# Performance work log

Hardware: AMD Instinct MI355X
Metric: run time of the kernel (lower is better)

## Reference

```python
import jax, jax.numpy as jnp
import numpy as np

WINDOW_SIZE = 11
SIGMA = 1.5
C1 = 0.01 ** 2
C2 = 0.03 ** 2


def _gaussian_window(window_size, sigma, channel):
    x = np.arange(window_size, dtype=np.float64)
    g = np.exp(-((x - window_size // 2) ** 2) / (2.0 * sigma ** 2))
    g = g / g.sum()
    w2d = np.outer(g, g).astype(np.float32)  # [K,K]
    # depthwise kernel: [C, 1, K, K] (OIHW with feature_group_count=C)
    return jnp.asarray(np.broadcast_to(w2d, (channel, 1, window_size, window_size)).copy())


def _depthwise_blur(x, window):
    pad = WINDOW_SIZE // 2
    return jax.lax.conv_general_dilated(
        x, window,
        window_strides=(1, 1),
        padding=[(pad, pad), (pad, pad)],
        feature_group_count=x.shape[1],
        dimension_numbers=('NCHW', 'OIHW', 'NCHW'))


def setup_inputs() -> dict:
    key = jax.random.key(0)
    k1, k2 = jax.random.split(key)
    shape = (16, 3, 512, 512)
    image = jax.random.uniform(k1, shape, dtype=jnp.float32)
    target = jax.random.uniform(k2, shape, dtype=jnp.float32)
    return {"image": image, "target": target}


def reference(image, target):
    channel = image.shape[1]
    window = _gaussian_window(WINDOW_SIZE, SIGMA, channel)

    mu1 = _depthwise_blur(image, window)
    mu2 = _depthwise_blur(target, window)
    mu1_sq = mu1 * mu1
    mu2_sq = mu2 * mu2
    mu1_mu2 = mu1 * mu2

    sigma1_sq = _depthwise_blur(image * image, window) - mu1_sq
    sigma2_sq = _depthwise_blur(target * target, window) - mu2_sq
    sigma12 = _depthwise_blur(image * target, window) - mu1_mu2

    ssim_map = ((2.0 * mu1_mu2 + C1) * (2.0 * sigma12 + C2)) / (
        (mu1_sq + mu2_sq + C1) * (sigma1_sq + sigma2_sq + C2))
    return 1.0 - jnp.mean(ssim_map)
```

## Files before the change

### kernel.cpp

```cpp
#include <hip/hip_runtime.h>
#include <hip/hip_fp16.h>
#include <math.h>


#define HH 512
#define WW 512
#define HW (HH*WW)
#define NPLANES 48
#define G_TILES 6
#define NBLOCKS 1024

typedef _Float16 f16x8 __attribute__((ext_vector_type(8)));
typedef _Float16 f16x4 __attribute__((ext_vector_type(4)));
typedef float f32x4 __attribute__((ext_vector_type(4)));

#define RAW_STRIDE 208
#define RAW_PLANE  9984
#define BUF_B      19968
#define LDS_TOTAL  39936

struct WParam { float A, B; };

__global__ void ssim_init_out(float* out) { out[0] = 1.0f; }

__device__ __forceinline__ void barrier_nodrain() {
    asm volatile("s_waitcnt lgkmcnt(0)" ::: "memory");
    __builtin_amdgcn_s_barrier();
    __builtin_amdgcn_sched_barrier(0);
}

__global__ __launch_bounds__(256, 4)
void ssim_mfma(const float* __restrict__ img, const float* __restrict__ tgt,
               float* __restrict__ out, WParam wp) {
    __shared__ alignas(16) char lds[LDS_TOTAL];
    __shared__ float wsum[4];

    const int tid  = threadIdx.x;
    const int wid  = tid >> 6;
    const int lane = tid & 63;
    const int cl   = lane & 15;
    const int am   = lane >> 4;

    const int it0 = tid,       ir0 = it0 / 10, ig0 = it0 - 10 * ir0;
    const int it1 = tid + 256, ir1 = it1 / 10, ig1 = it1 - 10 * ir1;
    const bool has1 = (tid < 164);

    float4 Xa[2], Xb[2], Ya[2], Yb[2];

    auto load_tile = [&](int tlin) {
        const int p   = tlin >> 7;
        const int rem = tlin & 127;
        const int R0  = (rem >> 3) * 32;
        const int C0  = (rem & 7) * 64;
        const float* ip = img + (size_t)p * HW;
        const float* tp = tgt + (size_t)p * HW;
        #pragma unroll
        for (int s = 0; s < 2; ++s) {
            if (s == 1 && !has1) break;
            int r   = s ? ir1 : ir0;
            int grp = s ? ig1 : ig0;
            int gr  = R0 - 5 + r;
            int gc0 = C0 - 8 + grp * 8;
            float4 xa = make_float4(0.f,0.f,0.f,0.f), xb = xa, ya = xa, yb = xa;
            if ((unsigned)gr < (unsigned)HH) {
                const float* xr = ip + (size_t)gr * WW;
                const float* yr = tp + (size_t)gr * WW;
                if ((unsigned)gc0 <= (unsigned)(WW - 4)) {
                    xa = *(const float4*)(xr + gc0);
                    ya = *(const float4*)(yr + gc0);
                }
                if ((unsigned)(gc0 + 4) <= (unsigned)(WW - 4)) {
                    xb = *(const float4*)(xr + gc0 + 4);
                    yb = *(const float4*)(yr + gc0 + 4);
                }
            }
            Xa[s] = xa; Xb[s] = xb; Ya[s] = ya; Yb[s] = yb;
        }
    };

    auto write_tile = [&](char* buf) {
        #pragma unroll
        for (int s = 0; s < 2; ++s) {
            if (s == 1 && !has1) break;
            int r   = s ? ir1 : ir0;
            int grp = s ? ig1 : ig0;
            f16x8 hx, hy;
            hx[0]=(_Float16)Xa[s].x; hx[1]=(_Float16)Xa[s].y;
            hx[2]=(_Float16)Xa[s].z; hx[3]=(_Float16)Xa[s].w;
            hx[4]=(_Float16)Xb[s].x; hx[5]=(_Float16)Xb[s].y;
            hx[6]=(_Float16)Xb[s].z; hx[7]=(_Float16)Xb[s].w;
            hy[0]=(_Float16)Ya[s].x; hy[1]=(_Float16)Ya[s].y;
            hy[2]=(_Float16)Ya[s].z; hy[3]=(_Float16)Ya[s].w;
            hy[4]=(_Float16)Yb[s].x; hy[5]=(_Float16)Yb[s].y;
            hy[6]=(_Float16)Yb[s].z; hy[7]=(_Float16)Yb[s].w;
            char* base = buf + r * RAW_STRIDE + grp * 16;
            *(f16x8*)(base + 0*RAW_PLANE) = hx;
            *(f16x8*)(base + 1*RAW_PLANE) = hy;
        }
    };

    const int base_t = blockIdx.x * G_TILES;
    load_tile(base_t);

    for (int i = tid; i < LDS_TOTAL / 4; i += 256)
        ((float*)lds)[i] = 0.f;

    f16x8 Bh;
    #pragma unroll
    for (int j = 0; j < 8; ++j) {
        int ih = 8*am + j - cl - 3;
        float t = (float)(ih - 5);
        Bh[j] = ((unsigned)ih <= 10u) ? (_Float16)(wp.A * exp2f(-wp.B*t*t))
                                      : (_Float16)0.f;
    }
    f16x4 Av1, Av2;
    #pragma unroll
    for (int j = 0; j < 4; ++j) {
        int k = 4*am + j;
        int i1 = k - cl;
        float t1 = (float)(i1 - 5);
        Av1[j] = ((unsigned)i1 <= 10u) ? (_Float16)(wp.A * exp2f(-wp.B*t1*t1))
                                       : (_Float16)0.f;
        int i2 = k + 16 - cl;
        float t2 = (float)(i2 - 5);
        Av2[j] = ((unsigned)i2 <= 10u) ? (_Float16)(wp.A * exp2f(-wp.B*t2*t2))
                                       : (_Float16)0.f;
    }
    __syncthreads();

    const float C1 = 1e-4f, C2 = 9e-4f;
    float lsum = 0.f;

    for (int g = 0; g < G_TILES; ++g) {
        char* buf = lds + (g & 1) * BUF_B;

        write_tile(buf);
        if (g + 1 < G_TILES) load_tile(base_t + g + 1);
        barrier_nodrain();

        {
            const int abase = cl * RAW_STRIDE + 32 * wid + am * 16;
            f16x8 hx3[3], hy3[3];
            #pragma unroll
            for (int mt = 0; mt < 3; ++mt) {
                hx3[mt] = *(const f16x8*)(buf + (16*mt) * RAW_STRIDE + abase);
                hy3[mt] = *(const f16x8*)(buf + RAW_PLANE + (16*mt) * RAW_STRIDE + abase);
            }

            f32x4 accv[4][2];
            #pragma unroll
            for (int q = 0; q < 4; ++q) {
                f32x4 Dh[3];
                #pragma unroll
                for (int mt = 0; mt < 3; ++mt) {
                    f16x8 A = (q == 0) ? hx3[mt]
                            : (q == 1) ? hy3[mt]
                            : (q == 2) ? (f16x8)(hx3[mt]*hx3[mt] + hy3[mt]*hy3[mt])
                                       : (f16x8)(hx3[mt]*hy3[mt]);
                    f32x4 zz = {0.f, 0.f, 0.f, 0.f};
                    Dh[mt] = __builtin_amdgcn_mfma_f32_16x16x32_f16(A, Bh, zz, 0, 0, 0);
                }
                #pragma unroll
                for (int mtv = 0; mtv < 2; ++mtv) {
                    f16x4 B1, B2;
                    #pragma unroll
                    for (int j = 0; j < 4; ++j) {
                        B1[j] = (_Float16)Dh[mtv][j];
                        B2[j] = (_Float16)Dh[mtv+1][j];
                    }
                    f32x4 zz = {0.f, 0.f, 0.f, 0.f};
                    f32x4 acc = __builtin_amdgcn_mfma_f32_16x16x16f16(Av2, B2, zz, 0, 0, 0);
                    accv[q][mtv] = __builtin_amdgcn_mfma_f32_16x16x16f16(Av1, B1, acc, 0, 0, 0);
                }
            }

            #pragma unroll
            for (int mtv = 0; mtv < 2; ++mtv) {
                #pragma unroll
                for (int j = 0; j < 4; ++j) {
                    float mu1 = accv[0][mtv][j], mu2 = accv[1][mtv][j];
                    float bss = accv[2][mtv][j], bxy = accv[3][mtv][j];
                    float mu1s = mu1*mu1, mu2s = mu2*mu2, mu12 = mu1*mu2;
                    float ssum = bss - mu1s - mu2s;
                    float s12  = bxy - mu12;
                    float num = (2.f*mu12 + C1) * (2.f*s12 + C2);
                    float den = (mu1s + mu2s + C1) * (ssum + C2);
                    lsum = fmaf(num, __builtin_amdgcn_rcpf(den), lsum);
                }
            }
        }
    }

    for (int off = 32; off > 0; off >>= 1)
        lsum += __shfl_down(lsum, off, 64);
    if (lane == 0) wsum[wid] = lsum;
    __syncthreads();
    if (tid == 0) {
        float bsum = wsum[0] + wsum[1] + wsum[2] + wsum[3];
        const float invN = 1.0f / (float)((size_t)NPLANES * HH * WW);
        atomicAdd(out, -bsum * invN);
    }
}

extern "C" void kernel_launch(void* const* d_in, const int* in_sizes, int n_in,
                              void* d_out, int out_size, void* d_ws, size_t ws_size,
                              hipStream_t stream) {
    const float* img = (const float*)d_in[0];
    const float* tgt = (const float*)d_in[1];
    float* out = (float*)d_out;

    double s = 0.0;
    for (int i = 0; i < 11; ++i) {
        double d = (double)(i - 5);
        s += exp(-(d * d) / 4.5);
    }
    WParam wp;
    wp.A = (float)(1.0 / s);
    wp.B = (float)(M_LOG2E / 4.5);

    ssim_init_out<<<1, 1, 0, stream>>>(out);
    ssim_mfma<<<NBLOCKS, 256, 0, stream>>>(img, tgt, out, wp);
}
```

Before: 40.28 us.

## Software-pipeline LDS fragment reads with ping-pong register sets across tiles

Unrolls the tile loop by two and keeps two register sets of A fragments, so the LDS reads for the next tile are issued before the MFMA work on the current tile. This is meant to hide LDS read latency behind compute. It also reorders the MFMA stages: all first-pass results are converted to f16 first, then the second pass and SSIM arithmetic run per output half, which shortens live accumulator ranges. The cost is higher register pressure from the duplicated fragments, which may hurt occupancy under the 4-waves launch bound.

```diff
diff --git a/kernel.cpp b/kernel.cpp
--- a/kernel.cpp
+++ b/kernel.cpp
@@ -130,66 +130,100 @@
 
     const float C1 = 1e-4f, C2 = 9e-4f;
     float lsum = 0.f;
-
-    for (int g = 0; g < G_TILES; ++g) {
-        char* buf = lds + (g & 1) * BUF_B;
-
-        write_tile(buf);
-        if (g + 1 < G_TILES) load_tile(base_t + g + 1);
-        barrier_nodrain();
-
-        {
-            const int abase = cl * RAW_STRIDE + 32 * wid + am * 16;
-            f16x8 hx3[3], hy3[3];
+    const int abase = cl * RAW_STRIDE + 32 * wid + am * 16;
+
+    f16x8 Ax0, Ax1, Ax2, Ay0, Ay1, Ay2;
+    f16x8 Bx0, Bx1, Bx2, By0, By1, By2;
+
+    auto read_frags_A = [&](const char* buf) {
+        Ax0 = *(const f16x8*)(buf + abase);
+        Ay0 = *(const f16x8*)(buf + RAW_PLANE + abase);
+        Ax1 = *(const f16x8*)(buf + 16 * RAW_STRIDE + abase);
+        Ay1 = *(const f16x8*)(buf + RAW_PLANE + 16 * RAW_STRIDE + abase);
+        Ax2 = *(const f16x8*)(buf + 32 * RAW_STRIDE + abase);
+        Ay2 = *(const f16x8*)(buf + RAW_PLANE + 32 * RAW_STRIDE + abase);
+    };
+    auto read_frags_B = [&](const char* buf) {
+        Bx0 = *(const f16x8*)(buf + abase);
+        By0 = *(const f16x8*)(buf + RAW_PLANE + abase);
+        Bx1 = *(const f16x8*)(buf + 16 * RAW_STRIDE + abase);
+        By1 = *(const f16x8*)(buf + RAW_PLANE + 16 * RAW_STRIDE + abase);
+        Bx2 = *(const f16x8*)(buf + 32 * RAW_STRIDE + abase);
+        By2 = *(const f16x8*)(buf + RAW_PLANE + 32 * RAW_STRIDE + abase);
+    };
+
+    auto compute = [&](f16x8 hx0, f16x8 hx1, f16x8 hx2,
+                       f16x8 hy0, f16x8 hy1, f16x8 hy2) {
+        f16x4 D16[4][3];
+        #pragma unroll
+        for (int q = 0; q < 4; ++q) {
             #pragma unroll
             for (int mt = 0; mt < 3; ++mt) {
-                hx3[mt] = *(const f16x8*)(buf + (16*mt) * RAW_STRIDE + abase);
-                hy3[mt] = *(const f16x8*)(buf + RAW_PLANE + (16*mt) * RAW_STRIDE + abase);
-            }
-
-            f32x4 accv[4][2];
+                f16x8 hxm = (mt == 0) ? hx0 : (mt == 1) ? hx1 : hx2;
+                f16x8 hym = (mt == 0) ? hy0 : (mt == 1) ? hy1 : hy2;
+                f16x8 A = (q == 0) ? hxm
+                        : (q == 1) ? hym
+                        : (q == 2) ? (f16x8)(hxm*hxm + hym*hym)
+                                   : (f16x8)(hxm*hym);
+                f32x4 zz = {0.f, 0.f, 0.f, 0.f};
+                f32x4 d = __builtin_amdgcn_mfma_f32_16x16x32_f16(A, Bh, zz, 0, 0, 0);
+                f16x4 h;
+                h[0]=(_Float16)d[0]; h[1]=(_Float16)d[1];
+                h[2]=(_Float16)d[2]; h[3]=(_Float16)d[3];
+                D16[q][mt] = h;
+            }
+        }
+        #pragma unroll
+        for (int mtv = 0; mtv < 2; ++mtv) {
+            f32x4 accv[4];
             #pragma unroll
             for (int q = 0; q < 4; ++q) {
-                f32x4 Dh[3];
-                #pragma unroll
-                for (int mt = 0; mt < 3; ++mt) {
-                    f16x8 A = (q == 0) ? hx3[mt]
-                            : (q == 1) ? hy3[mt]
-                            : (q == 2) ? (f16x8)(hx3[mt]*hx3[mt] + hy3[mt]*hy3[mt])
-                                       : (f16x8)(hx3[mt]*hy3[mt]);
-                    f32x4 zz = {0.f, 0.f, 0.f, 0.f};
-                    Dh[mt] = __builtin_amdgcn_mfma_f32_16x16x32_f16(A, Bh, zz, 0, 0, 0);
-                }
-                #pragma unroll
-                for (int mtv = 0; mtv < 2; ++mtv) {
-                    f16x4 B1, B2;
-                    #pragma unroll
-                    for (int j = 0; j < 4; ++j) {
-                        B1[j] = (_Float16)Dh[mtv][j];
-                        B2[j] = (_Float16)Dh[mtv+1][j];
-                    }
-                    f32x4 zz = {0.f, 0.f, 0.f, 0.f};
-                    f32x4 acc = __builtin_amdgcn_mfma_f32_16x16x16f16(Av2, B2, zz, 0, 0, 0);
-                    accv[q][mtv] = __builtin_amdgcn_mfma_f32_16x16x16f16(Av1, B1, acc, 0, 0, 0);
-                }
-            }
-
+                f32x4 zz = {0.f, 0.f, 0.f, 0.f};
+                f32x4 a = __builtin_amdgcn_mfma_f32_16x16x16f16(
+                              Av2, D16[q][mtv+1], zz, 0, 0, 0);
+                accv[q] = __builtin_amdgcn_mfma_f32_16x16x16f16(
+                              Av1, D16[q][mtv], a, 0, 0, 0);
+            }
             #pragma unroll
-            for (int mtv = 0; mtv < 2; ++mtv) {
-                #pragma unroll
-                for (int j = 0; j < 4; ++j) {
-                    float mu1 = accv[0][mtv][j], mu2 = accv[1][mtv][j];
-                    float bss = accv[2][mtv][j], bxy = accv[3][mtv][j];
-                    float mu1s = mu1*mu1, mu2s = mu2*mu2, mu12 = mu1*mu2;
-                    float ssum = bss - mu1s - mu2s;
-                    float s12  = bxy - mu12;
-                    float num = (2.f*mu12 + C1) * (2.f*s12 + C2);
-                    float den = (mu1s + mu2s + C1) * (ssum + C2);
-                    lsum = fmaf(num, __builtin_amdgcn_rcpf(den), lsum);
-                }
-            }
-        }
-    }
+            for (int j = 0; j < 4; ++j) {
+                float mu1 = accv[0][j], mu2 = accv[1][j];
+                float bss = accv[2][j], bxy = accv[3][j];
+                float mu1s = mu1*mu1, mu2s = mu2*mu2, mu12 = mu1*mu2;
+                float ssum = bss - mu1s - mu2s;
+                float s12  = bxy - mu12;
+                float num = (2.f*mu12 + C1) * (2.f*s12 + C2);
+                float den = (mu1s + mu2s + C1) * (ssum + C2);
+                lsum = fmaf(num, __builtin_amdgcn_rcpf(den), lsum);
+            }
+        }
+    };
+
+    char* buf0 = lds;
+    char* buf1 = lds + BUF_B;
+
+    write_tile(buf0);
+    load_tile(base_t + 1);
+    barrier_nodrain();
+    read_frags_A(buf0);
+
+    #pragma unroll 1
+    for (int gp = 0; gp < G_TILES / 2 - 1; ++gp) {
+        write_tile(buf1);
+        load_tile(base_t + 2*gp + 2);
+        barrier_nodrain();
+        read_frags_B(buf1);
+        compute(Ax0, Ax1, Ax2, Ay0, Ay1, Ay2);
+        write_tile(buf0);
+        if (2*gp + 3 < G_TILES) load_tile(base_t + 2*gp + 3);
+        barrier_nodrain();
+        read_frags_A(buf0);
+        compute(Bx0, Bx1, Bx2, By0, By1, By2);
+    }
+    write_tile(buf1);
+    barrier_nodrain();
+    read_frags_B(buf1);
+    compute(Ax0, Ax1, Ax2, Ay0, Ay1, Ay2);
+    compute(Bx0, Bx1, Bx2, By0, By1, By2);
 
     for (int off = 32; off > 0; off >>= 1)
         lsum += __shfl_down(lsum, off, 64);
```

Measured after the change: 43.69 us. 8.5% more time.
